# Optimization experiments

Hardware: AMD Instinct MI355X
Metric: run time of the kernel (lower is better)

The kernel has to match this reference:

```python
import jax, jax.numpy as jnp
import numpy as np

C = 128      # in = out channels
H = 4        # heads
HD = C // H  # head dim
N_DRUG, N_DIS, E = 50000, 20000, 250000
EA_DIM = 8


def _seg_softmax(logits, seg, n):
    # torch_geometric.utils.softmax: per-destination-node softmax over incident edges
    m = jax.ops.segment_max(logits, seg, num_segments=n)          # [n,H]
    ex = jnp.exp(logits - m[seg])
    s = jax.ops.segment_sum(ex, seg, num_segments=n)
    return ex / (s[seg] + 1e-16)


def _edge_conv(src_x, dst_x, si, di, Ws, bs, Wd, bd, attn, gate, n_dst):
    msg_src = src_x[si] @ Ws + bs           # [E,C] gather + linear
    msg_dst = dst_x[di] @ Wd + bd
    msg = msg_src + msg_dst
    if gate is not None:
        msg = msg * gate
    e = msg.shape[0]
    mh = msg.reshape(e, H, HD)
    sh = msg_src.reshape(e, H, HD)
    dh = msg_dst.reshape(e, H, HD)
    logits = (sh * dh).sum(-1) / jnp.sqrt(jnp.float32(HD)) + (mh * attn).sum(-1)  # [E,H]
    w = _seg_softmax(logits, di, n_dst)
    out = (mh * w[..., None]).reshape(e, C)
    return jax.ops.segment_sum(out, di, num_segments=n_dst)      # [n_dst,C]


def setup_inputs() -> dict:
    key = jax.random.key(0)
    ks = jax.random.split(key, 24)
    s = 1.0 / np.sqrt(C)
    d = {
        'x_drug': jax.random.normal(ks[0], (N_DRUG, C), jnp.float32),
        'x_disease': jax.random.normal(ks[1], (N_DIS, C), jnp.float32),
        'ea_treats': jax.random.normal(ks[2], (E, EA_DIM), jnp.float32),
        'si_t': jax.random.randint(ks[3], (E,), 0, N_DRUG),
        'di_t': jax.random.randint(ks[4], (E,), 0, N_DIS),
        'si_r': jax.random.randint(ks[5], (E,), 0, N_DIS),
        'di_r': jax.random.randint(ks[6], (E,), 0, N_DRUG),
        'Ws_t': jax.random.normal(ks[7], (C, C), jnp.float32) * s,
        'bs_t': jnp.zeros((C,), jnp.float32),
        'Wd_t': jax.random.normal(ks[8], (C, C), jnp.float32) * s,
        'bd_t': jnp.zeros((C,), jnp.float32),
        'attn_t': jax.random.normal(ks[9], (1, H, HD), jnp.float32) * 0.1,
        'Wg1': jax.random.normal(ks[10], (EA_DIM, C), jnp.float32) * (1.0 / np.sqrt(EA_DIM)),
        'bg1': jnp.zeros((C,), jnp.float32),
        'Wg2': jax.random.normal(ks[11], (C, C), jnp.float32) * s,
        'bg2': jnp.zeros((C,), jnp.float32),
        'Ws_r': jax.random.normal(ks[12], (C, C), jnp.float32) * s,
        'bs_r': jnp.zeros((C,), jnp.float32),
        'Wd_r': jax.random.normal(ks[13], (C, C), jnp.float32) * s,
        'bd_r': jnp.zeros((C,), jnp.float32),
        'attn_r': jax.random.normal(ks[14], (1, H, HD), jnp.float32) * 0.1,
        'Wo_drug': jax.random.normal(ks[15], (C, C), jnp.float32) * s,
        'bo_drug': jnp.zeros((C,), jnp.float32),
        'Wo_dis': jax.random.normal(ks[16], (C, C), jnp.float32) * s,
        'bo_dis': jnp.zeros((C,), jnp.float32),
    }
    return d


def reference(x_drug, x_disease, ea_treats, si_t, di_t, si_r, di_r,
              Ws_t, bs_t, Wd_t, bd_t, attn_t, Wg1, bg1, Wg2, bg2,
              Ws_r, bs_r, Wd_r, bd_r, attn_r,
              Wo_drug, bo_drug, Wo_dis, bo_dis):
    # edge gate for (drug, treats, disease): continuous edge attrs -> Linear-GELU-Linear-Sigmoid
    gate = jax.nn.sigmoid(jax.nn.gelu(ea_treats @ Wg1 + bg1, approximate=False) @ Wg2 + bg2)
    aggr_dis = _edge_conv(x_drug, x_disease, si_t, di_t, Ws_t, bs_t, Wd_t, bd_t, attn_t, gate, N_DIS)
    aggr_drug = _edge_conv(x_disease, x_drug, si_r, di_r, Ws_r, bs_r, Wd_r, bd_r, attn_r, None, N_DRUG)
    # single message per node type -> mean is identity; then per-node-type lin_out
    out_drug = aggr_drug @ Wo_drug + bo_drug
    out_dis = aggr_dis @ Wo_dis + bo_dis
    return out_drug, out_dis
```

## Files before the change

kernel.cpp:

```cpp
#include <hip/hip_runtime.h>
#include <hip/hip_bf16.h>
#include <math.h>

#define N_DRUG 50000
#define N_DIS  20000
#define NE     250000
#define NE_PAD 250048

#define NB0 79
#define NBT 275

typedef __bf16 bf16x8 __attribute__((ext_vector_type(8)));
typedef __bf16 bf16x4 __attribute__((ext_vector_type(4)));
typedef __bf16 bf16x2 __attribute__((ext_vector_type(2)));
typedef float  f32x4  __attribute__((ext_vector_type(4)));
typedef float  f32x2  __attribute__((ext_vector_type(2)));

__device__ __forceinline__ bf16x8 bz8() {
  bf16x8 v;
  #pragma unroll
  for (int j = 0; j < 8; ++j) v[j] = (__bf16)0.f;
  return v;
}

__device__ __forceinline__ float gelu_fast(float x) {
  float ax = fabsf(x);
  float t = fmaf(ax, 0.019527f, 3.43654e-4f);
  t = fmaf(ax, t, 0.1151945f);
  t = fmaf(ax, t, 0.1968564f);
  float p = fmaf(ax, t, 1.0f);
  float p2 = p * p;
  float p4 = p2 * p2;
  float r = __builtin_amdgcn_rcpf(p4);
  float sel = (x >= 0.f) ? (2.0f - r) : r;
  return 0.5f * x * sel;
}

__device__ __forceinline__ float sigmoid_fast(float v) {
  return __builtin_amdgcn_rcpf(1.0f + __expf(-v));
}

struct Seg {
  const void* A[4];
  const float* W[4];
  const float* bias[4];
  void* out[4];
  int M[4];
  int bstart[5];
};

template <int AIN_BF16, int OUT_BF16>
__global__ __launch_bounds__(256)
void gemm_seg(Seg d)
{
  __shared__ __bf16 Wt[128][136];

  const int b = blockIdx.x;
  const int sidx = (b >= d.bstart[3]) ? 3 : (b >= d.bstart[2]) ? 2
                 : (b >= d.bstart[1]) ? 1 : 0;
  const int nb = d.bstart[sidx + 1] - d.bstart[sidx];
  const int lb = b - d.bstart[sidx];
  const float* W = d.W[sidx];
  const float* bias = d.bias[sidx];
  const int M = d.M[sidx];
  const int ntiles = (M + 63) >> 6;
  const int tid = threadIdx.x;
  const int wv = tid >> 6, lane = tid & 63;
  const int m16 = lane & 15, quad = lane >> 4;

  for (int idx = tid; idx < 16384; idx += 256) {
    int k = idx >> 7, n = idx & 127;
    Wt[n][k] = (__bf16)W[idx];
  }
  __syncthreads();

  float bv[8];
  #pragma unroll
  for (int ct = 0; ct < 8; ++ct) bv[ct] = bias[ct * 16 + m16];

  auto load_afr = [&](int t, bf16x8* afr) {
    const int arow = (t << 6) + wv * 16 + m16;
    const bool ok = (t < ntiles) && (arow < M);
    if (AIN_BF16) {
      const __bf16* ap = (const __bf16*)d.A[sidx] + (long)arow * 128 + quad * 8;
      #pragma unroll
      for (int kt = 0; kt < 4; ++kt)
        afr[kt] = ok ? *(const bf16x8*)(ap + kt * 32) : bz8();
    } else {
      const float* ap = (const float*)d.A[sidx] + (long)arow * 128 + quad * 8;
      #pragma unroll
      for (int kt = 0; kt < 4; ++kt) {
        bf16x8 v = bz8();
        if (ok) {
          f32x4 lo = *(const f32x4*)(ap + kt * 32);
          f32x4 hi = *(const f32x4*)(ap + kt * 32 + 4);
          #pragma unroll
          for (int j = 0; j < 4; ++j) { v[j] = (__bf16)lo[j]; v[4 + j] = (__bf16)hi[j]; }
        }
        afr[kt] = v;
      }
    }
  };

  bf16x8 afr[4];
  if (lb < ntiles) load_afr(lb, afr);

  for (int t = lb; t < ntiles; t += nb) {
    bf16x8 nafr[4];
    load_afr(t + nb, nafr);

    f32x4 acc[8];
    #pragma unroll
    for (int ct = 0; ct < 8; ++ct) acc[ct] = (f32x4){0.f, 0.f, 0.f, 0.f};
    #pragma unroll
    for (int kt = 0; kt < 4; ++kt) {
      #pragma unroll
      for (int ct = 0; ct < 8; ++ct) {
        bf16x8 bfr = *(const bf16x8*)&Wt[ct * 16 + m16][kt * 32 + quad * 8];
        acc[ct] = __builtin_amdgcn_mfma_f32_16x16x32_bf16(afr[kt], bfr, acc[ct], 0, 0, 0);
      }
    }

    const int rb = (t << 6) + wv * 16 + quad * 4;
    #pragma unroll
    for (int ct = 0; ct < 8; ++ct) {
      const int col = ct * 16 + m16;
      #pragma unroll
      for (int rg = 0; rg < 4; ++rg) {
        int gr = rb + rg;
        if (gr < M) {
          float v = acc[ct][rg] + bv[ct];
          if (OUT_BF16) ((__bf16*)d.out[sidx])[(long)gr * 128 + col] = (__bf16)v;
          else          ((float*)d.out[sidx])[(long)gr * 128 + col] = v;
        }
      }
    }
    #pragma unroll
    for (int kt = 0; kt < 4; ++kt) afr[kt] = nafr[kt];
  }
}

__global__ __launch_bounds__(256)
void gate_kernel(const float* __restrict__ EA, const float* __restrict__ W2,
                 const float* __restrict__ Wg1, const float* __restrict__ bg1,
                 const float* __restrict__ bg2, __bf16* __restrict__ out)
{
  __shared__ __bf16 Wt[128][136];
  __shared__ __bf16 H[64][136];
  const int tid = threadIdx.x;
  const int wv = tid >> 6, lane = tid & 63;
  const int m16 = lane & 15, quad = lane >> 4;

  for (int idx = tid; idx < 16384; idx += 256) {
    int k = idx >> 7, n = idx & 127;
    Wt[n][k] = (__bf16)W2[idx];
  }
  __syncthreads();

  bf16x8 b1[8];
  #pragma unroll
  for (int ct = 0; ct < 8; ++ct) {
    bf16x8 v = bz8();
    if (quad == 0) {
      #pragma unroll
      for (int j = 0; j < 8; ++j) v[j] = (__bf16)Wg1[j * 128 + ct * 16 + m16];
    }
    b1[ct] = v;
  }
  float b1v[8], b2v[8];
  #pragma unroll
  for (int ct = 0; ct < 8; ++ct) {
    b1v[ct] = bg1[ct * 16 + m16];
    b2v[ct] = bg2[ct * 16 + m16];
  }

  const int ntiles = (NE + 63) >> 6;
  const int hr = wv * 16 + quad * 4;
  const int ar = wv * 16 + m16;

  for (int t = blockIdx.x; t < ntiles; t += gridDim.x) {
    const int r0 = t << 6;
    const int arow = r0 + wv * 16 + m16;

    bf16x8 a1 = bz8();
    if (quad == 0 && arow < NE) {
      f32x4 e0 = *(const f32x4*)(EA + (long)arow * 8);
      f32x4 e1 = *(const f32x4*)(EA + (long)arow * 8 + 4);
      #pragma unroll
      for (int j = 0; j < 4; ++j) { a1[j] = (__bf16)e0[j]; a1[4 + j] = (__bf16)e1[j]; }
    }
    f32x4 h[8];
    #pragma unroll
    for (int ct = 0; ct < 8; ++ct)
      h[ct] = __builtin_amdgcn_mfma_f32_16x16x32_bf16(a1, b1[ct], (f32x4){0.f,0.f,0.f,0.f}, 0, 0, 0);

    #pragma unroll
    for (int ct = 0; ct < 8; ++ct) {
      const int col = ct * 16 + m16;
      #pragma unroll
      for (int rg = 0; rg < 4; ++rg)
        H[hr + rg][col] = (__bf16)gelu_fast(h[ct][rg] + b1v[ct]);
    }
    asm volatile("s_waitcnt lgkmcnt(0)" ::: "memory");

    bf16x8 afr[4];
    #pragma unroll
    for (int kt = 0; kt < 4; ++kt)
      afr[kt] = *(const bf16x8*)&H[ar][kt * 32 + quad * 8];
    asm volatile("" ::: "memory");

    f32x4 acc[8];
    #pragma unroll
    for (int ct = 0; ct < 8; ++ct) acc[ct] = (f32x4){0.f, 0.f, 0.f, 0.f};
    #pragma unroll
    for (int kt = 0; kt < 4; ++kt) {
      #pragma unroll
      for (int ct = 0; ct < 8; ++ct) {
        bf16x8 bfr = *(const bf16x8*)&Wt[ct * 16 + m16][kt * 32 + quad * 8];
        acc[ct] = __builtin_amdgcn_mfma_f32_16x16x32_bf16(afr[kt], bfr, acc[ct], 0, 0, 0);
      }
    }

    #pragma unroll
    for (int ct = 0; ct < 8; ++ct) {
      const int col = ct * 16 + m16;
      #pragma unroll
      for (int rg = 0; rg < 4; ++rg)
        H[hr + rg][col] = (__bf16)sigmoid_fast(acc[ct][rg] + b2v[ct]);
    }
    asm volatile("s_waitcnt lgkmcnt(0)" ::: "memory");

    bf16x8 gout[4];
    #pragma unroll
    for (int kt = 0; kt < 4; ++kt)
      gout[kt] = *(const bf16x8*)&H[ar][kt * 32 + quad * 8];
    asm volatile("" ::: "memory");

    __bf16* op = out + (long)arow * 128 + quad * 8;
    #pragma unroll
    for (int kt = 0; kt < 4; ++kt)
      *(bf16x8*)(op + kt * 32) = gout[kt];
  }
}

__global__ __launch_bounds__(256)
void histo2(const int* __restrict__ di_t, const int* __restrict__ di_r,
            int* __restrict__ cnt_dis, int* __restrict__ cnt_drug, int half) {
  int b = blockIdx.x;
  if (b < half) {
    int i = b * 256 + threadIdx.x;
    if (i < NE) atomicAdd(&cnt_dis[di_t[i]], 1);
  } else {
    int i = (b - half) * 256 + threadIdx.x;
    if (i < NE) atomicAdd(&cnt_drug[di_r[i]], 1);
  }
}

__global__ __launch_bounds__(256)
void scatter2(const int* __restrict__ di_t, const int* __restrict__ di_r,
              int* __restrict__ cur_dis, int* __restrict__ cur_drug,
              int* __restrict__ sorted_t, int* __restrict__ sorted_r, int half) {
  int b = blockIdx.x;
  if (b < half) {
    int i = b * 256 + threadIdx.x;
    if (i < NE) sorted_t[atomicAdd(&cur_dis[di_t[i]], 1)] = i;
  } else {
    int i = (b - half) * 256 + threadIdx.x;
    if (i < NE) sorted_r[atomicAdd(&cur_drug[di_r[i]], 1)] = i;
  }
}

__device__ __forceinline__ void seg_geom(int b, int& base, int& n, int& lb) {
  if (b < NB0) { base = 0;     n = 20000; lb = b; }
  else         { base = 20000; n = 50000; lb = b - NB0; }
}

__global__ __launch_bounds__(256)
void scan_partial(const int* __restrict__ cnt, int* __restrict__ bsum) {
  __shared__ int sh[256];
  int b = blockIdx.x, t = threadIdx.x;
  int base, n, lb; seg_geom(b, base, n, lb);
  int i = lb * 256 + t;
  sh[t] = (i < n) ? cnt[base + i] : 0;
  __syncthreads();
  for (int d = 1; d < 256; d <<= 1) {
    int vv = (t >= d) ? sh[t - d] : 0;
    __syncthreads();
    sh[t] += vv;
    __syncthreads();
  }
  if (t == 255) bsum[b] = sh[255];
}

__global__ __launch_bounds__(512)
void scan_block(const int* __restrict__ bsum, int* __restrict__ bexc) {
  __shared__ int v[512];
  __shared__ int f[512];
  int t = threadIdx.x;
  int own = (t < NBT) ? bsum[t] : 0;
  v[t] = own;
  f[t] = (t == 0 || t == NB0 || t >= NBT) ? 1 : 0;
  __syncthreads();
  for (int d = 1; d < 512; d <<= 1) {
    int vv = 0, ff = 1;
    if (t >= d) { vv = v[t - d]; ff = f[t - d]; }
    __syncthreads();
    if (t >= d && !f[t]) { v[t] += vv; f[t] |= ff; }
    __syncthreads();
  }
  if (t < NBT) bexc[t] = v[t] - own;
}

__global__ __launch_bounds__(256)
void scan_final(const int* __restrict__ cnt, const int* __restrict__ bexc,
                int* __restrict__ offs, int* __restrict__ cursor) {
  __shared__ int sh[256];
  int b = blockIdx.x, t = threadIdx.x;
  int base, n, lb; seg_geom(b, base, n, lb);
  int i = lb * 256 + t;
  int own = (i < n) ? cnt[base + i] : 0;
  sh[t] = own;
  __syncthreads();
  for (int d = 1; d < 256; d <<= 1) {
    int vv = (t >= d) ? sh[t - d] : 0;
    __syncthreads();
    sh[t] += vv;
    __syncthreads();
  }
  int off = bexc[b] + sh[t] - own;
  if (i < n) { offs[base + i] = off; cursor[base + i] = off; }
}

template <int HASGATE>
__global__ __launch_bounds__(256)
void aggregate(const __bf16* __restrict__ Xs, const __bf16* __restrict__ Xd,
               const int* __restrict__ si, const int* __restrict__ sorted,
               const int* __restrict__ offs, const int* __restrict__ cnt,
               const __bf16* __restrict__ gate, const float* __restrict__ attn,
               __bf16* __restrict__ out, int n)
{
  int w = (int)((blockIdx.x * 256 + threadIdx.x) >> 6);
  if (w >= n) return;
  const int lane = threadIdx.x & 63;
  const int c = lane * 2;

  f32x2 at = *(const f32x2*)(attn + c);
  bf16x2 xdb = *(const bf16x2*)(Xd + (long)w * 128 + c);
  const float xd0 = (float)xdb[0], xd1 = (float)xdb[1];
  const int start = offs[w];
  const int m = cnt[w];

  float n0 = 0.f, n1 = 0.f, den = 0.f;

  bf16x2 xs_n = {(__bf16)0.f, (__bf16)0.f};
  bf16x2 g_n  = {(__bf16)0.f, (__bf16)0.f};
  if (m > 0) {
    int e = sorted[start];
    int s = si[e];
    xs_n = *(const bf16x2*)(Xs + (long)s * 128 + c);
    if (HASGATE) g_n = *(const bf16x2*)(gate + (long)e * 128 + c);
  }
  for (int j = 0; j < m; ++j) {
    bf16x2 xsb = xs_n, gb = g_n;
    if (j + 1 < m) {
      int e = sorted[start + j + 1];
      int s = si[e];
      xs_n = *(const bf16x2*)(Xs + (long)s * 128 + c);
      if (HASGATE) g_n = *(const bf16x2*)(gate + (long)e * 128 + c);
    }
    float xs0 = (float)xsb[0], xs1 = (float)xsb[1];
    float m0 = xs0 + xd0, m1 = xs1 + xd1;
    if (HASGATE) { m0 *= (float)gb[0]; m1 *= (float)gb[1]; }
    float part = (xs0 * xd0 + xs1 * xd1) * 0.17677669529663687f
               + m0 * at[0] + m1 * at[1];
    part += __shfl_xor(part, 1);
    part += __shfl_xor(part, 2);
    part += __shfl_xor(part, 4);
    part += __shfl_xor(part, 8);
    float ex = __expf(part);
    n0 += m0 * ex;
    n1 += m1 * ex;
    den += ex;
  }

  float r = __builtin_amdgcn_rcpf(den + 1e-16f);
  bf16x2 o;
  o[0] = (__bf16)(n0 * r);
  o[1] = (__bf16)(n1 * r);
  *(bf16x2*)(out + (long)w * 128 + c) = o;
}

extern "C" void kernel_launch(void* const* d_in, const int* in_sizes, int n_in,
                              void* d_out, int out_size, void* d_ws, size_t ws_size,
                              hipStream_t stream)
{
  const float* x_drug  = (const float*)d_in[0];
  const float* x_dis   = (const float*)d_in[1];
  const float* ea      = (const float*)d_in[2];
  const int*   si_t    = (const int*)d_in[3];
  const int*   di_t    = (const int*)d_in[4];
  const int*   si_r    = (const int*)d_in[5];
  const int*   di_r    = (const int*)d_in[6];
  const float* Ws_t    = (const float*)d_in[7];
  const float* bs_t    = (const float*)d_in[8];
  const float* Wd_t    = (const float*)d_in[9];
  const float* bd_t    = (const float*)d_in[10];
  const float* attn_t  = (const float*)d_in[11];
  const float* Wg1     = (const float*)d_in[12];
  const float* bg1     = (const float*)d_in[13];
  const float* Wg2     = (const float*)d_in[14];
  const float* bg2     = (const float*)d_in[15];
  const float* Ws_r    = (const float*)d_in[16];
  const float* bs_r    = (const float*)d_in[17];
  const float* Wd_r    = (const float*)d_in[18];
  const float* bd_r    = (const float*)d_in[19];
  const float* attn_r  = (const float*)d_in[20];
  const float* Wo_drug = (const float*)d_in[21];
  const float* bo_drug = (const float*)d_in[22];
  const float* Wo_dis  = (const float*)d_in[23];
  const float* bo_dis  = (const float*)d_in[24];

  __bf16* wsb      = (__bf16*)d_ws;
  __bf16* Xs_t     = wsb;
  __bf16* Xd_t     = Xs_t + 6400000;
  __bf16* Xs_r     = Xd_t + 2560000;
  __bf16* Xd_r     = Xs_r + 2560000;
  __bf16* aggr_dis = Xd_r + 6400000;
  __bf16* gate     = aggr_dis + 2560000;
  int* cnt_dis    = (int*)(gate + (long)NE_PAD * 128);
  int* cnt_drug   = cnt_dis + 20000;
  int* offs_dis   = cnt_drug + 50000;
  int* offs_drug  = offs_dis + 20000;
  int* cur_dis    = offs_drug + 50000;
  int* cur_drug   = cur_dis + 20000;
  int* sorted_t   = cur_drug + 50000;
  int* sorted_r   = sorted_t + 250000;
  int* bsum       = sorted_r + 250000;
  int* bexc       = bsum + 512;

  __bf16* aggr_drug = Xs_t;

  float* out_drug = (float*)d_out;
  float* out_dis  = out_drug + (long)N_DRUG * 128;

  hipMemsetAsync(cnt_dis, 0, 70000 * sizeof(int), stream);

  const int eb = (NE + 255) / 256;

  histo2<<<2 * eb, 256, 0, stream>>>(di_t, di_r, cnt_dis, cnt_drug, eb);
  scan_partial<<<NBT, 256, 0, stream>>>(cnt_dis, bsum);
  scan_block<<<1, 512, 0, stream>>>(bsum, bexc);
  scan_final<<<NBT, 256, 0, stream>>>(cnt_dis, bexc, offs_dis, cur_dis);
  scatter2<<<2 * eb, 256, 0, stream>>>(di_t, di_r, cur_dis, cur_drug, sorted_t, sorted_r, eb);

  Seg nd;
  nd.A[0] = x_drug; nd.W[0] = Ws_t; nd.bias[0] = bs_t; nd.out[0] = Xs_t; nd.M[0] = N_DRUG;
  nd.A[1] = x_dis;  nd.W[1] = Wd_t; nd.bias[1] = bd_t; nd.out[1] = Xd_t; nd.M[1] = N_DIS;
  nd.A[2] = x_dis;  nd.W[2] = Ws_r; nd.bias[2] = bs_r; nd.out[2] = Xs_r; nd.M[2] = N_DIS;
  nd.A[3] = x_drug; nd.W[3] = Wd_r; nd.bias[3] = bd_r; nd.out[3] = Xd_r; nd.M[3] = N_DRUG;
  nd.bstart[0] = 0; nd.bstart[1] = 274; nd.bstart[2] = 384; nd.bstart[3] = 494; nd.bstart[4] = 768;
  gemm_seg<0, 1><<<768, 256, 0, stream>>>(nd);

  gate_kernel<<<512, 256, 0, stream>>>(ea, Wg2, Wg1, bg1, bg2, gate);

  aggregate<1><<<(N_DIS + 3) / 4,  256, 0, stream>>>(Xs_t, Xd_t, si_t, sorted_t, offs_dis,  cnt_dis,  gate,    attn_t, aggr_dis,  N_DIS);
  aggregate<0><<<(N_DRUG + 3) / 4, 256, 0, stream>>>(Xs_r, Xd_r, si_r, sorted_r, offs_drug, cnt_drug, nullptr, attn_r, aggr_drug, N_DRUG);

  Seg od;
  od.A[0] = aggr_drug; od.W[0] = Wo_drug; od.bias[0] = bo_drug; od.out[0] = out_drug; od.M[0] = N_DRUG;
  od.A[1] = aggr_dis;  od.W[1] = Wo_dis;  od.bias[1] = bo_dis;  od.out[1] = out_dis;  od.M[1] = N_DIS;
  od.A[2] = od.A[1];   od.W[2] = od.W[1]; od.bias[2] = od.bias[1]; od.out[2] = od.out[1]; od.M[2] = N_DIS;
  od.A[3] = od.A[1];   od.W[3] = od.W[1]; od.bias[3] = od.bias[1]; od.out[3] = od.out[1]; od.M[3] = N_DIS;
  od.bstart[0] = 0; od.bstart[1] = 548; od.bstart[2] = 768; od.bstart[3] = 768; od.bstart[4] = 768;
  gemm_seg<1, 0><<<768, 256, 0, stream>>>(od);
}
```

Measured before the change: 382.1 us.

## Presort gate and source indices by destination, merge aggregate kernels with 4-way prefetch

The scatter pass now writes source node indices in destination-sorted order, and the gate kernel computes gates directly in sorted edge order. The aggregate step can then read source ids and gate rows contiguously instead of going through a double indirection. The two aggregate launches are merged into a single kernel, and its edge loop is unrolled by four with four-deep prefetch to hide gather latency. Cost: gate_kernel now does a scattered read of edge attributes, and the dis/drug branch in the merged kernel may diverge at the boundary.

```diff
diff --git a/kernel.cpp b/kernel.cpp
--- a/kernel.cpp
+++ b/kernel.cpp
@@ -143,7 +143,8 @@
 __global__ __launch_bounds__(256)
 void gate_kernel(const float* __restrict__ EA, const float* __restrict__ W2,
                  const float* __restrict__ Wg1, const float* __restrict__ bg1,
-                 const float* __restrict__ bg2, __bf16* __restrict__ out)
+                 const float* __restrict__ bg2, const int* __restrict__ sorted_t,
+                 __bf16* __restrict__ out)
 {
   __shared__ __bf16 Wt[128][136];
   __shared__ __bf16 H[64][136];
@@ -179,13 +180,13 @@
   const int ar = wv * 16 + m16;
 
   for (int t = blockIdx.x; t < ntiles; t += gridDim.x) {
-    const int r0 = t << 6;
-    const int arow = r0 + wv * 16 + m16;
+    const int p = (t << 6) + wv * 16 + m16;
 
     bf16x8 a1 = bz8();
-    if (quad == 0 && arow < NE) {
-      f32x4 e0 = *(const f32x4*)(EA + (long)arow * 8);
-      f32x4 e1 = *(const f32x4*)(EA + (long)arow * 8 + 4);
+    if (quad == 0 && p < NE) {
+      int e = sorted_t[p];
+      f32x4 e0 = *(const f32x4*)(EA + (long)e * 8);
+      f32x4 e1 = *(const f32x4*)(EA + (long)e * 8 + 4);
       #pragma unroll
       for (int j = 0; j < 4; ++j) { a1[j] = (__bf16)e0[j]; a1[4 + j] = (__bf16)e1[j]; }
     }
@@ -236,7 +237,7 @@
       gout[kt] = *(const bf16x8*)&H[ar][kt * 32 + quad * 8];
     asm volatile("" ::: "memory");
 
-    __bf16* op = out + (long)arow * 128 + quad * 8;
+    __bf16* op = out + (long)p * 128 + quad * 8;
     #pragma unroll
     for (int kt = 0; kt < 4; ++kt)
       *(bf16x8*)(op + kt * 32) = gout[kt];
@@ -258,15 +259,24 @@
 
 __global__ __launch_bounds__(256)
 void scatter2(const int* __restrict__ di_t, const int* __restrict__ di_r,
+              const int* __restrict__ si_t, const int* __restrict__ si_r,
               int* __restrict__ cur_dis, int* __restrict__ cur_drug,
-              int* __restrict__ sorted_t, int* __restrict__ sorted_r, int half) {
+              int* __restrict__ sorted_t, int* __restrict__ ssrc_t,
+              int* __restrict__ ssrc_r, int half) {
   int b = blockIdx.x;
   if (b < half) {
     int i = b * 256 + threadIdx.x;
-    if (i < NE) sorted_t[atomicAdd(&cur_dis[di_t[i]], 1)] = i;
+    if (i < NE) {
+      int p = atomicAdd(&cur_dis[di_t[i]], 1);
+      sorted_t[p] = i;
+      ssrc_t[p] = si_t[i];
+    }
   } else {
     int i = (b - half) * 256 + threadIdx.x;
-    if (i < NE) sorted_r[atomicAdd(&cur_drug[di_r[i]], 1)] = i;
+    if (i < NE) {
+      int p = atomicAdd(&cur_drug[di_r[i]], 1);
+      ssrc_r[p] = si_r[i];
+    }
   }
 }
 
@@ -331,63 +341,91 @@
   if (i < n) { offs[base + i] = off; cursor[base + i] = off; }
 }
 
-template <int HASGATE>
-__global__ __launch_bounds__(256)
-void aggregate(const __bf16* __restrict__ Xs, const __bf16* __restrict__ Xd,
-               const int* __restrict__ si, const int* __restrict__ sorted,
-               const int* __restrict__ offs, const int* __restrict__ cnt,
-               const __bf16* __restrict__ gate, const float* __restrict__ attn,
-               __bf16* __restrict__ out, int n)
+__global__ __launch_bounds__(256)
+void aggregate2(const __bf16* __restrict__ Xs_t, const __bf16* __restrict__ Xd_t,
+                const __bf16* __restrict__ Xs_r, const __bf16* __restrict__ Xd_r,
+                const int* __restrict__ ssrc_t, const int* __restrict__ ssrc_r,
+                const int* __restrict__ offs, const int* __restrict__ cnt,
+                const __bf16* __restrict__ gate_s,
+                const float* __restrict__ attn_t, const float* __restrict__ attn_r,
+                __bf16* __restrict__ aggr_dis, __bf16* __restrict__ aggr_drug)
 {
-  int w = (int)((blockIdx.x * 256 + threadIdx.x) >> 6);
-  if (w >= n) return;
+  const int gw = (int)((blockIdx.x * 256 + threadIdx.x) >> 6);
+  if (gw >= N_DIS + N_DRUG) return;
   const int lane = threadIdx.x & 63;
   const int c = lane * 2;
+  const bool isDis = gw < N_DIS;
+  const int node = isDis ? gw : gw - N_DIS;
+  const __bf16* Xs = isDis ? Xs_t : Xs_r;
+  const __bf16* Xd = isDis ? Xd_t : Xd_r;
+  const int* ssrc = isDis ? ssrc_t : ssrc_r;
+  const float* attn = isDis ? attn_t : attn_r;
+  __bf16* outp = isDis ? aggr_dis : aggr_drug;
 
   f32x2 at = *(const f32x2*)(attn + c);
-  bf16x2 xdb = *(const bf16x2*)(Xd + (long)w * 128 + c);
+  bf16x2 xdb = *(const bf16x2*)(Xd + (long)node * 128 + c);
   const float xd0 = (float)xdb[0], xd1 = (float)xdb[1];
-  const int start = offs[w];
-  const int m = cnt[w];
+  const int start = offs[gw];
+  const int m = cnt[gw];
 
   float n0 = 0.f, n1 = 0.f, den = 0.f;
-
-  bf16x2 xs_n = {(__bf16)0.f, (__bf16)0.f};
-  bf16x2 g_n  = {(__bf16)0.f, (__bf16)0.f};
-  if (m > 0) {
-    int e = sorted[start];
-    int s = si[e];
-    xs_n = *(const bf16x2*)(Xs + (long)s * 128 + c);
-    if (HASGATE) g_n = *(const bf16x2*)(gate + (long)e * 128 + c);
-  }
-  for (int j = 0; j < m; ++j) {
-    bf16x2 xsb = xs_n, gb = g_n;
-    if (j + 1 < m) {
-      int e = sorted[start + j + 1];
-      int s = si[e];
-      xs_n = *(const bf16x2*)(Xs + (long)s * 128 + c);
-      if (HASGATE) g_n = *(const bf16x2*)(gate + (long)e * 128 + c);
-    }
-    float xs0 = (float)xsb[0], xs1 = (float)xsb[1];
-    float m0 = xs0 + xd0, m1 = xs1 + xd1;
-    if (HASGATE) { m0 *= (float)gb[0]; m1 *= (float)gb[1]; }
-    float part = (xs0 * xd0 + xs1 * xd1) * 0.17677669529663687f
-               + m0 * at[0] + m1 * at[1];
-    part += __shfl_xor(part, 1);
-    part += __shfl_xor(part, 2);
-    part += __shfl_xor(part, 4);
-    part += __shfl_xor(part, 8);
-    float ex = __expf(part);
-    n0 += m0 * ex;
-    n1 += m1 * ex;
-    den += ex;
+  const bf16x2 z2 = {(__bf16)0.f, (__bf16)0.f};
+
+  bf16x2 xa[4], ga[4];
+  #pragma unroll
+  for (int u = 0; u < 4; ++u) {
+    xa[u] = z2; ga[u] = z2;
+    if (u < m) {
+      int s = ssrc[start + u];
+      xa[u] = *(const bf16x2*)(Xs + (long)s * 128 + c);
+      if (isDis) ga[u] = *(const bf16x2*)(gate_s + (long)(start + u) * 128 + c);
+    }
+  }
+
+  for (int j = 0; j < m; j += 4) {
+    bf16x2 xb[4], gb[4];
+    #pragma unroll
+    for (int u = 0; u < 4; ++u) {
+      xb[u] = z2; gb[u] = z2;
+      int jn = j + 4 + u;
+      if (jn < m) {
+        int s = ssrc[start + jn];
+        xb[u] = *(const bf16x2*)(Xs + (long)s * 128 + c);
+        if (isDis) gb[u] = *(const bf16x2*)(gate_s + (long)(start + jn) * 128 + c);
+      }
+    }
+
+    float part[4], mm0[4], mm1[4];
+    #pragma unroll
+    for (int u = 0; u < 4; ++u) {
+      float xs0 = (float)xa[u][0], xs1 = (float)xa[u][1];
+      float m0 = xs0 + xd0, m1 = xs1 + xd1;
+      if (isDis) { m0 *= (float)ga[u][0]; m1 *= (float)ga[u][1]; }
+      mm0[u] = m0; mm1[u] = m1;
+      part[u] = (xs0 * xd0 + xs1 * xd1) * 0.17677669529663687f
+              + m0 * at[0] + m1 * at[1];
+    }
+    #pragma unroll
+    for (int dd = 1; dd <= 8; dd <<= 1) {
+      #pragma unroll
+      for (int u = 0; u < 4; ++u) part[u] += __shfl_xor(part[u], dd);
+    }
+    #pragma unroll
+    for (int u = 0; u < 4; ++u) {
+      float ex = (j + u < m) ? __expf(part[u]) : 0.f;
+      n0 += mm0[u] * ex;
+      n1 += mm1[u] * ex;
+      den += ex;
+    }
+    #pragma unroll
+    for (int u = 0; u < 4; ++u) { xa[u] = xb[u]; ga[u] = gb[u]; }
   }
 
   float r = __builtin_amdgcn_rcpf(den + 1e-16f);
   bf16x2 o;
   o[0] = (__bf16)(n0 * r);
   o[1] = (__bf16)(n1 * r);
-  *(bf16x2*)(out + (long)w * 128 + c) = o;
+  *(bf16x2*)(outp + (long)node * 128 + c) = o;
 }
 
 extern "C" void kernel_launch(void* const* d_in, const int* in_sizes, int n_in,
@@ -425,8 +463,7 @@
   __bf16* Xd_t     = Xs_t + 6400000;
   __bf16* Xs_r     = Xd_t + 2560000;
   __bf16* Xd_r     = Xs_r + 2560000;
-  __bf16* aggr_dis = Xd_r + 6400000;
-  __bf16* gate     = aggr_dis + 2560000;
+  __bf16* gate     = Xd_r + 6400000;
   int* cnt_dis    = (int*)(gate + (long)NE_PAD * 128);
   int* cnt_drug   = cnt_dis + 20000;
   int* offs_dis   = cnt_drug + 50000;
@@ -434,11 +471,13 @@
   int* cur_dis    = offs_drug + 50000;
   int* cur_drug   = cur_dis + 20000;
   int* sorted_t   = cur_drug + 50000;
-  int* sorted_r   = sorted_t + 250000;
-  int* bsum       = sorted_r + 250000;
+  int* ssrc_t     = sorted_t + 250000;
+  int* ssrc_r     = ssrc_t + 250000;
+  int* bsum       = ssrc_r + 250000;
   int* bexc       = bsum + 512;
 
-  __bf16* aggr_drug = Xs_t;
+  __bf16* aggr_dis  = Xd_t;
+  __bf16* aggr_drug = Xd_r;
 
   float* out_drug = (float*)d_out;
   float* out_dis  = out_drug + (long)N_DRUG * 128;
@@ -451,7 +490,8 @@
   scan_partial<<<NBT, 256, 0, stream>>>(cnt_dis, bsum);
   scan_block<<<1, 512, 0, stream>>>(bsum, bexc);
   scan_final<<<NBT, 256, 0, stream>>>(cnt_dis, bexc, offs_dis, cur_dis);
-  scatter2<<<2 * eb, 256, 0, stream>>>(di_t, di_r, cur_dis, cur_drug, sorted_t, sorted_r, eb);
+  scatter2<<<2 * eb, 256, 0, stream>>>(di_t, di_r, si_t, si_r, cur_dis, cur_drug,
+                                       sorted_t, ssrc_t, ssrc_r, eb);
 
   Seg nd;
   nd.A[0] = x_drug; nd.W[0] = Ws_t; nd.bias[0] = bs_t; nd.out[0] = Xs_t; nd.M[0] = N_DRUG;
@@ -461,10 +501,11 @@
   nd.bstart[0] = 0; nd.bstart[1] = 274; nd.bstart[2] = 384; nd.bstart[3] = 494; nd.bstart[4] = 768;
   gemm_seg<0, 1><<<768, 256, 0, stream>>>(nd);
 
-  gate_kernel<<<512, 256, 0, stream>>>(ea, Wg2, Wg1, bg1, bg2, gate);
-
-  aggregate<1><<<(N_DIS + 3) / 4,  256, 0, stream>>>(Xs_t, Xd_t, si_t, sorted_t, offs_dis,  cnt_dis,  gate,    attn_t, aggr_dis,  N_DIS);
-  aggregate<0><<<(N_DRUG + 3) / 4, 256, 0, stream>>>(Xs_r, Xd_r, si_r, sorted_r, offs_drug, cnt_drug, nullptr, attn_r, aggr_drug, N_DRUG);
+  gate_kernel<<<512, 256, 0, stream>>>(ea, Wg2, Wg1, bg1, bg2, sorted_t, gate);
+
+  aggregate2<<<(N_DIS + N_DRUG + 3) / 4, 256, 0, stream>>>(
+      Xs_t, Xd_t, Xs_r, Xd_r, ssrc_t, ssrc_r, offs_dis, cnt_dis,
+      gate, attn_t, attn_r, aggr_dis, aggr_drug);
 
   Seg od;
   od.A[0] = aggr_drug; od.W[0] = Wo_drug; od.bias[0] = bo_drug; od.out[0] = out_drug; od.M[0] = N_DRUG;
```

Result: faster. 339.5 us (-11.1%).
